# Optimization experiments

Measured on AMD Instinct MI355X. Metric: run time of the kernel, lower is better.

## Reference

```python
import jax, jax.numpy as jnp
import numpy as np

ROPE_THETA = 10000.0

def rope(x):
    # RoPE over the FULL model_dim (applied pre head-split, as in the source),
    # interleaved even/odd pairs. x: [B, S, D]
    B, S, D = x.shape
    half = D // 2
    inv_freq = 1.0 / (ROPE_THETA ** (jnp.arange(half, dtype=jnp.float32) * 2.0 / D))
    ang = jnp.arange(S, dtype=jnp.float32)[:, None] * inv_freq[None, :]  # [S, half]
    cos, sin = jnp.cos(ang), jnp.sin(ang)
    x1, x2 = x[..., 0::2], x[..., 1::2]
    r1 = x1 * cos - x2 * sin
    r2 = x1 * sin + x2 * cos
    return jnp.stack([r1, r2], axis=-1).reshape(B, S, D)


def setup_inputs() -> dict:
    key = jax.random.key(0)
    ks = jax.random.split(key, 9)
    B, S, D = 4, 2048, 768
    w = 0.02
    return {
        "X":  jax.random.normal(ks[0], (B, S, D), dtype=jnp.float32),
        "Wq": jax.random.normal(ks[1], (D, D), dtype=jnp.float32) * w,
        "bq": jnp.zeros((D,), dtype=jnp.float32),
        "Wk": jax.random.normal(ks[2], (D, D), dtype=jnp.float32) * w,
        "bk": jnp.zeros((D,), dtype=jnp.float32),
        "Wv": jax.random.normal(ks[3], (D, D), dtype=jnp.float32) * w,
        "bv": jnp.zeros((D,), dtype=jnp.float32),
        "Wo": jax.random.normal(ks[4], (D, D), dtype=jnp.float32) * w,
        "bo": jnp.zeros((D,), dtype=jnp.float32),
    }


def reference(X, Wq, bq, Wk, bk, Wv, bv, Wo, bo):
    NUM_HEADS = 12
    B, S, D = X.shape
    hd = D // NUM_HEADS

    q = rope(X @ Wq + bq)   # RoPE applied pre-split on full model_dim
    k = rope(X @ Wk + bk)
    v = X @ Wv + bv

    # Contiguous per-head slices == reshape to [B, S, H, hd]
    qh = q.reshape(B, S, NUM_HEADS, hd)
    kh = k.reshape(B, S, NUM_HEADS, hd)
    vh = v.reshape(B, S, NUM_HEADS, hd)

    scores = jnp.einsum('bqhd,bkhd->bhqk', qh, kh) / jnp.sqrt(jnp.float32(hd))
    causal = jnp.tril(jnp.ones((S, S), dtype=bool))
    scores = jnp.where(causal[None, None, :, :], scores, -jnp.inf)
    weights = jax.nn.softmax(scores, axis=-1)
    out = jnp.einsum('bhqk,bkhd->bqhd', weights, vh).reshape(B, S, D)
    return out @ Wo + bo
```

## Files before the change

### kernel.cpp

```cpp
#include <hip/hip_runtime.h>
#include <math.h>

#define D_MODEL 768
#define NUM_HEADS 12
#define HEAD_DIM 64
#define SEQ 2048
#define BATCH 4
#define MROWS (BATCH * SEQ)
#define HALF_D (D_MODEL / 2)

typedef __bf16 bf16x8 __attribute__((ext_vector_type(8)));
typedef __bf16 bf16x4 __attribute__((ext_vector_type(4)));
typedef float  f32x4  __attribute__((ext_vector_type(4)));

__device__ __forceinline__ void gload_lds16(const void* gp, void* lp) {
    __builtin_amdgcn_global_load_lds(
        (const __attribute__((address_space(1))) unsigned int*)gp,
        (__attribute__((address_space(3))) unsigned int*)lp, 16, 0, 0);
}

__global__ __launch_bounds__(256)
void rope_table(float2* __restrict__ tab)
{
    int idx = blockIdx.x * 256 + threadIdx.x;
    int s = idx / HALF_D;
    int j = idx - s * HALF_D;
    float freq = __expf(-(float)j * (9.210340371976184f / 384.0f));
    float ang  = (float)s * freq;
    float sn, cs;
    sincosf(ang, &sn, &cs);
    tab[idx] = make_float2(cs, sn);
}

__global__ __launch_bounds__(256)
void cast_x(const float* __restrict__ X, __bf16* __restrict__ Xb)
{
    size_t i = ((size_t)blockIdx.x * 256 + threadIdx.x) * 8;
    float4 u = *(const float4*)(X + i);
    float4 v = *(const float4*)(X + i + 4);
    bf16x8 o;
    o[0]=(__bf16)u.x; o[1]=(__bf16)u.y; o[2]=(__bf16)u.z; o[3]=(__bf16)u.w;
    o[4]=(__bf16)v.x; o[5]=(__bf16)v.y; o[6]=(__bf16)v.z; o[7]=(__bf16)v.w;
    *(bf16x8*)(Xb + i) = o;
}

__global__ __launch_bounds__(256)
void wcast(const float* __restrict__ W0, const float* __restrict__ W1,
           const float* __restrict__ W2, const float* __restrict__ W3,
           __bf16* __restrict__ T0, __bf16* __restrict__ T1,
           __bf16* __restrict__ T2, __bf16* __restrict__ T3)
{
    __shared__ float t[64][65];
    const int z = blockIdx.z;
    const float* W = z == 0 ? W0 : z == 1 ? W1 : z == 2 ? W2 : W3;
    __bf16*      T = z == 0 ? T0 : z == 1 ? T1 : z == 2 ? T2 : T3;

    const int tid = threadIdx.x;
    const int r0 = blockIdx.y * 64, c0 = blockIdx.x * 64;
    const int lx = tid & 63, g = tid >> 6;

    #pragma unroll
    for (int rr = 0; rr < 16; ++rr) {
        int r = g * 16 + rr;
        t[r][lx] = W[(size_t)(r0 + r) * D_MODEL + c0 + lx];
    }
    __syncthreads();

    const int n  = tid >> 2;
    const int kb = (tid & 3) * 16;
    bf16x8 o1, o2;
    #pragma unroll
    for (int m = 0; m < 8; ++m) o1[m] = (__bf16)t[kb + m][n];
    #pragma unroll
    for (int m = 0; m < 8; ++m) o2[m] = (__bf16)t[kb + 8 + m][n];
    __bf16* dst = T + (size_t)(c0 + n) * D_MODEL + r0 + kb;
    *(bf16x8*)dst       = o1;
    *(bf16x8*)(dst + 8) = o2;
}

__global__ __launch_bounds__(256)
void qkv_gemm(const __bf16* __restrict__ Xb,
              const __bf16* __restrict__ Wqt, const __bf16* __restrict__ Wkt,
              const __bf16* __restrict__ Wvt,
              const float* __restrict__ bq, const float* __restrict__ bk,
              const float* __restrict__ bv,
              const float2* __restrict__ tab,
              __bf16* __restrict__ Qb, __bf16* __restrict__ Kb,
              __bf16* __restrict__ Vtb)
{
    __shared__ bf16x8 Asf[2][8][64];
    __shared__ bf16x8 Bsf[2][8][64];

    const int tid  = threadIdx.x;
    const int wv   = tid >> 6;
    const int ln   = tid & 63;
    const int t15  = ln & 15;
    const int quad = ln >> 4;
    const int wr = wv >> 1, wc = wv & 1;

    const int lin = blockIdx.x;
    const int c   = lin >> 6;
    const int r   = lin & 63;
    const int which = c / 6;
    const int col0  = (c % 6) * 128;
    const int row0  = r * 128;

    const __bf16* Wt  = which == 0 ? Wqt : which == 1 ? Wkt : Wvt;
    const float* bias = which == 0 ? bq  : which == 1 ? bk  : bv;

    f32x4 acc[4][4];
    #pragma unroll
    for (int i = 0; i < 4; ++i)
        #pragma unroll
        for (int j = 0; j < 4; ++j) acc[i][j] = (f32x4){0.f,0.f,0.f,0.f};

    const __bf16* a0 = Xb + (size_t)(row0 + 16 * wv       + t15) * D_MODEL + 8 * quad;
    const __bf16* a1 = Xb + (size_t)(row0 + 16 * (wv + 4) + t15) * D_MODEL + 8 * quad;
    const __bf16* b0 = Wt + (size_t)(col0 + 16 * wv       + t15) * D_MODEL + 8 * quad;
    const __bf16* b1 = Wt + (size_t)(col0 + 16 * (wv + 4) + t15) * D_MODEL + 8 * quad;

    for (int k0 = 0; k0 < D_MODEL; k0 += 64) {
        __syncthreads();
        #pragma unroll
        for (int ks = 0; ks < 2; ++ks) {
            const int kk = k0 + 32 * ks;
            gload_lds16(a0 + kk, &Asf[ks][wv][0]);
            gload_lds16(a1 + kk, &Asf[ks][wv + 4][0]);
            gload_lds16(b0 + kk, &Bsf[ks][wv][0]);
            gload_lds16(b1 + kk, &Bsf[ks][wv + 4][0]);
        }
        __syncthreads();

        #pragma unroll
        for (int ks = 0; ks < 2; ++ks) {
            bf16x8 af[4], bfr[4];
            #pragma unroll
            for (int i = 0; i < 4; ++i) af[i]  = Asf[ks][4 * wr + i][ln];
            #pragma unroll
            for (int j = 0; j < 4; ++j) bfr[j] = Bsf[ks][4 * wc + j][ln];
            #pragma unroll
            for (int i = 0; i < 4; ++i)
                #pragma unroll
                for (int j = 0; j < 4; ++j)
                    acc[i][j] = __builtin_amdgcn_mfma_f32_16x16x32_bf16(af[i], bfr[j], acc[i][j], 0, 0, 0);
        }
    }

    #pragma unroll
    for (int i = 0; i < 4; ++i) {
        const int rowb = row0 + 64 * wr + 16 * i + 4 * quad;
        #pragma unroll
        for (int j = 0; j < 4; ++j) {
            const int col = col0 + 64 * wc + 16 * j + t15;
            const float bval = bias[col];
            if (which < 2) {
                const int jh  = col >> 1;
                const float sgn = (col & 1) ? 1.0f : -1.0f;
                const float oscale = (which == 0) ? 0.125f : 1.0f;
                __bf16* dst = (which ? Kb : Qb);
                #pragma unroll
                for (int rr = 0; rr < 4; ++rr) {
                    const int rw = rowb + rr;
                    const int s  = rw & (SEQ - 1);
                    float val  = acc[i][j][rr] + bval;
                    float part = __shfl_xor(val, 1, 64);
                    float2 cs  = tab[(size_t)s * HALF_D + jh];
                    dst[(size_t)rw * D_MODEL + col] = (__bf16)((val * cs.x + part * sgn * cs.y) * oscale);
                }
            } else {
                const int h = col >> 6, d = col & 63;
                const int bidx = rowb >> 11, s = rowb & (SEQ - 1);
                bf16x4 pk;
                #pragma unroll
                for (int rr = 0; rr < 4; ++rr) pk[rr] = (__bf16)(acc[i][j][rr] + bval);
                *(bf16x4*)(Vtb + ((size_t)(bidx * NUM_HEADS + h) * 64 + d) * SEQ + s) = pk;
            }
        }
    }
}

__global__ __launch_bounds__(256)
void out_gemm(const __bf16* __restrict__ Ab, const __bf16* __restrict__ Wt,
              const float* __restrict__ bias, float* __restrict__ Cout)
{
    __shared__ bf16x8 Asf[2][8][64];
    __shared__ bf16x8 Bsf[2][8][64];

    const int tid  = threadIdx.x;
    const int wv   = tid >> 6;
    const int ln   = tid & 63;
    const int t15  = ln & 15;
    const int quad = ln >> 4;
    const int wr = wv >> 1, wc = wv & 1;

    const int lin = blockIdx.x;
    const int col0 = (lin >> 6) * 128;
    const int row0 = (lin & 63) * 128;

    f32x4 acc[4][4];
    #pragma unroll
    for (int i = 0; i < 4; ++i)
        #pragma unroll
        for (int j = 0; j < 4; ++j) acc[i][j] = (f32x4){0.f,0.f,0.f,0.f};

    const __bf16* a0 = Ab + (size_t)(row0 + 16 * wv       + t15) * D_MODEL + 8 * quad;
    const __bf16* a1 = Ab + (size_t)(row0 + 16 * (wv + 4) + t15) * D_MODEL + 8 * quad;
    const __bf16* b0 = Wt + (size_t)(col0 + 16 * wv       + t15) * D_MODEL + 8 * quad;
    const __bf16* b1 = Wt + (size_t)(col0 + 16 * (wv + 4) + t15) * D_MODEL + 8 * quad;

    for (int k0 = 0; k0 < D_MODEL; k0 += 64) {
        __syncthreads();
        #pragma unroll
        for (int ks = 0; ks < 2; ++ks) {
            const int kk = k0 + 32 * ks;
            gload_lds16(a0 + kk, &Asf[ks][wv][0]);
            gload_lds16(a1 + kk, &Asf[ks][wv + 4][0]);
            gload_lds16(b0 + kk, &Bsf[ks][wv][0]);
            gload_lds16(b1 + kk, &Bsf[ks][wv + 4][0]);
        }
        __syncthreads();

        #pragma unroll
        for (int ks = 0; ks < 2; ++ks) {
            bf16x8 af[4], bfr[4];
            #pragma unroll
            for (int i = 0; i < 4; ++i) af[i]  = Asf[ks][4 * wr + i][ln];
            #pragma unroll
            for (int j = 0; j < 4; ++j) bfr[j] = Bsf[ks][4 * wc + j][ln];
            #pragma unroll
            for (int i = 0; i < 4; ++i)
                #pragma unroll
                for (int j = 0; j < 4; ++j)
                    acc[i][j] = __builtin_amdgcn_mfma_f32_16x16x32_bf16(af[i], bfr[j], acc[i][j], 0, 0, 0);
        }
    }

    #pragma unroll
    for (int i = 0; i < 4; ++i) {
        const int rowb = row0 + 64 * wr + 16 * i + 4 * quad;
        #pragma unroll
        for (int j = 0; j < 4; ++j) {
            const int col = col0 + 64 * wc + 16 * j + t15;
            const float bval = bias[col];
            #pragma unroll
            for (int rr = 0; rr < 4; ++rr)
                Cout[(size_t)(rowb + rr) * D_MODEL + col] = acc[i][j][rr] + bval;
        }
    }
}

__device__ __forceinline__ void attn_tile(
    const bf16x8 (*Kbuf)[64], const bf16x8 (*Vbuf)[64],
    __bf16 (*Psw)[72],
    bf16x8 aq0, bf16x8 aq1,
    f32x4* o, float* lacc,
    int ln, int t15, int quad, int j0, int qabs, bool domask)
{
    f32x4 s[4];
    #pragma unroll
    for (int c = 0; c < 4; ++c) {
        s[c] = (f32x4){0.f, 0.f, 0.f, 0.f};
        s[c] = __builtin_amdgcn_mfma_f32_16x16x32_bf16(aq0, Kbuf[c][ln],     s[c], 0, 0, 0);
        s[c] = __builtin_amdgcn_mfma_f32_16x16x32_bf16(aq1, Kbuf[4 + c][ln], s[c], 0, 0, 0);
    }

    float p[4][4];
    #pragma unroll
    for (int c = 0; c < 4; ++c)
        #pragma unroll
        for (int r = 0; r < 4; ++r) {
            float e = __expf(s[c][r]);
            if (domask && (j0 + 16 * c + t15 > qabs + r)) e = 0.f;
            p[c][r] = e;
            lacc[r] += e;
        }

    #pragma unroll
    for (int c = 0; c < 4; ++c)
        #pragma unroll
        for (int r = 0; r < 4; ++r)
            Psw[4 * quad + r][16 * c + t15] = (__bf16)p[c][r];
    __asm__ volatile("s_waitcnt lgkmcnt(0)" ::: "memory");

    bf16x8 ap0 = *(const bf16x8*)&Psw[t15][8 * quad];
    bf16x8 ap1 = *(const bf16x8*)&Psw[t15][32 + 8 * quad];

    #pragma unroll
    for (int c = 0; c < 4; ++c) {
        o[c] = __builtin_amdgcn_mfma_f32_16x16x32_bf16(ap0, Vbuf[c][ln],     o[c], 0, 0, 0);
        o[c] = __builtin_amdgcn_mfma_f32_16x16x32_bf16(ap1, Vbuf[4 + c][ln], o[c], 0, 0, 0);
    }
}

__global__ __launch_bounds__(512)
void attn_flash(const __bf16* __restrict__ Q, const __bf16* __restrict__ K,
                const __bf16* __restrict__ Vt, __bf16* __restrict__ O)
{
    __shared__ bf16x8 Kf[2][8][64];
    __shared__ bf16x8 Vf[2][8][64];
    __shared__ __bf16 Psb[8][16][72];

    const int tid  = threadIdx.x;
    const int wv   = tid >> 6;
    const int ln   = tid & 63;
    const int t15  = ln & 15;
    const int quad = ln >> 4;

    const int n  = blockIdx.x;
    const int sb = n >> 8;
    const int tb = n & 255;
    const int a  = tb & 15;
    const int qt = (sb == 0) ? a : (sb == 1) ? (15 - a) : ((a + 8) & 15);
    const int bh = (tb >> 4) + 16 * sb;
    const int b  = bh / NUM_HEADS;
    const int h  = bh % NUM_HEADS;
    const int q0 = qt * 128;
    const int nt = (q0 >> 6) + 2;

    bf16x8 aq0, aq1;
    {
        const __bf16* qs = Q + (size_t)(b * SEQ + q0 + 16 * wv + t15) * D_MODEL + h * 64 + 8 * quad;
        aq0 = *(const bf16x8*)qs;
        aq1 = *(const bf16x8*)(qs + 32);
    }

    const __bf16* kp = K  + ((size_t)b * SEQ + 16 * (wv & 3) + t15) * D_MODEL
                          + h * 64 + 32 * (wv >> 2) + 8 * quad;
    const __bf16* vp = Vt + ((size_t)bh * 64 + 16 * (wv & 3) + t15) * SEQ
                          + 32 * (wv >> 2) + 8 * quad;

    f32x4 o[4];
    #pragma unroll
    for (int c = 0; c < 4; ++c) o[c] = (f32x4){0.f,0.f,0.f,0.f};
    float lacc[4] = {0.f, 0.f, 0.f, 0.f};
    const int qabs = q0 + 16 * wv + 4 * quad;

    gload_lds16(kp, &Kf[0][wv][0]);
    gload_lds16(vp, &Vf[0][wv][0]);

    int cur = 0;
    for (int it = 0; it < nt; ++it) {
        __syncthreads();
        if (it + 1 < nt) {
            const int jn = (it + 1) * 64;
            gload_lds16(kp + (size_t)jn * D_MODEL, &Kf[cur ^ 1][wv][0]);
            gload_lds16(vp + jn,                   &Vf[cur ^ 1][wv][0]);
        }
        const int j0 = it * 64;
        const bool domask = (j0 + 63) > (q0 + 16 * wv);
        attn_tile(Kf[cur], Vf[cur], Psb[wv], aq0, aq1, o, lacc,
                  ln, t15, quad, j0, qabs, domask);
        cur ^= 1;
    }

    #pragma unroll
    for (int off = 1; off < 16; off <<= 1)
        #pragma unroll
        for (int r = 0; r < 4; ++r)
            lacc[r] += __shfl_xor(lacc[r], off, 64);

    float inv[4];
    #pragma unroll
    for (int r = 0; r < 4; ++r) inv[r] = 1.0f / lacc[r];
    #pragma unroll
    for (int c = 0; c < 4; ++c)
        #pragma unroll
        for (int r = 0; r < 4; ++r) {
            int row = qabs + r;
            O[(size_t)(b * SEQ + row) * D_MODEL + h * 64 + 16 * c + t15] = (__bf16)(o[c][r] * inv[r]);
        }
}

extern "C" void kernel_launch(void* const* d_in, const int* in_sizes, int n_in,
                              void* d_out, int out_size, void* d_ws, size_t ws_size,
                              hipStream_t stream) {
    const float* X  = (const float*)d_in[0];
    const float* Wq = (const float*)d_in[1];
    const float* bq = (const float*)d_in[2];
    const float* Wk = (const float*)d_in[3];
    const float* bk = (const float*)d_in[4];
    const float* Wv = (const float*)d_in[5];
    const float* bv = (const float*)d_in[6];
    const float* Wo = (const float*)d_in[7];
    const float* bo = (const float*)d_in[8];
    float* out = (float*)d_out;

    const size_t BSD = (size_t)MROWS * D_MODEL;
    const size_t WSZ = (size_t)D_MODEL * D_MODEL;

    __bf16* Xb  = (__bf16*)d_ws;
    __bf16* Qb  = Xb  + BSD;
    __bf16* Kb  = Qb  + BSD;
    __bf16* Vtb = Kb  + BSD;
    __bf16* Ob  = Vtb + BSD;
    __bf16* Wqt = Ob  + BSD;
    __bf16* Wkt = Wqt + WSZ;
    __bf16* Wvt = Wkt + WSZ;
    __bf16* Wot = Wvt + WSZ;
    float2* Tab = (float2*)(Wot + WSZ);

    rope_table<<<(SEQ * HALF_D) / 256, 256, 0, stream>>>(Tab);
    cast_x<<<BSD / (256 * 8), 256, 0, stream>>>(X, Xb);
    wcast<<<dim3(12, 12, 4), 256, 0, stream>>>(Wq, Wk, Wv, Wo, Wqt, Wkt, Wvt, Wot);

    qkv_gemm<<<1152, 256, 0, stream>>>(Xb, Wqt, Wkt, Wvt, bq, bk, bv, Tab, Qb, Kb, Vtb);

    attn_flash<<<768, 512, 0, stream>>>(Qb, Kb, Vtb, Ob);

    out_gemm<<<384, 256, 0, stream>>>(Ob, Wot, bo, out);
}
```

Measured before the change: 275.1 us.

## Restructure QKV GEMM to stage full-K A tile in LDS and stream B from registers

The QKV projection GEMM now uses 32x256 output tiles. Each block loads its whole 32-row by 768-K slab of X into LDS once, behind a single barrier. Each wave then streams its 64 columns of the transposed weight straight from global memory into registers with a three-slot prefetch ring, which removes the per-K-step LDS round trips and barriers. The grid doubles to 2304 blocks. In exchange, A-tile reuse per weight load drops and each block holds 48 KB of LDS, which may limit occupancy, and weight reads now rely on cache rather than shared staging.

Measured after the change: 312.5 us. +13.6%, slower.

```diff
diff --git a/kernel.cpp b/kernel.cpp
--- a/kernel.cpp
+++ b/kernel.cpp
@@ -88,70 +88,74 @@
               __bf16* __restrict__ Qb, __bf16* __restrict__ Kb,
               __bf16* __restrict__ Vtb)
 {
-    __shared__ bf16x8 Asf[2][8][64];
-    __shared__ bf16x8 Bsf[2][8][64];
+    __shared__ bf16x8 Af[48][64];
 
     const int tid  = threadIdx.x;
     const int wv   = tid >> 6;
     const int ln   = tid & 63;
     const int t15  = ln & 15;
     const int quad = ln >> 4;
-    const int wr = wv >> 1, wc = wv & 1;
-
-    const int lin = blockIdx.x;
-    const int c   = lin >> 6;
-    const int r   = lin & 63;
-    const int which = c / 6;
-    const int col0  = (c % 6) * 128;
-    const int row0  = r * 128;
+
+    const int lin  = blockIdx.x;
+    const int c    = lin >> 8;
+    const int r    = lin & 255;
+    const int which = c / 3;
+    const int col0  = (c % 3) * 256;
+    const int row0  = r * 32;
 
     const __bf16* Wt  = which == 0 ? Wqt : which == 1 ? Wkt : Wvt;
     const float* bias = which == 0 ? bq  : which == 1 ? bk  : bv;
 
-    f32x4 acc[4][4];
-    #pragma unroll
-    for (int i = 0; i < 4; ++i)
+    #pragma unroll
+    for (int cc = 0; cc < 12; ++cc) {
+        const int id = wv * 12 + cc;
+        const int s  = id >> 1;
+        const int i  = id & 1;
+        const __bf16* src = Xb + (size_t)(row0 + 16 * i + t15) * D_MODEL + 32 * s + 8 * quad;
+        gload_lds16(src, &Af[id][0]);
+    }
+    __syncthreads();
+
+    const __bf16* Bbase = Wt + (size_t)(col0 + 64 * wv + t15) * D_MODEL + 8 * quad;
+
+    f32x4 acc[2][4];
+    #pragma unroll
+    for (int i = 0; i < 2; ++i)
         #pragma unroll
         for (int j = 0; j < 4; ++j) acc[i][j] = (f32x4){0.f,0.f,0.f,0.f};
 
-    const __bf16* a0 = Xb + (size_t)(row0 + 16 * wv       + t15) * D_MODEL + 8 * quad;
-    const __bf16* a1 = Xb + (size_t)(row0 + 16 * (wv + 4) + t15) * D_MODEL + 8 * quad;
-    const __bf16* b0 = Wt + (size_t)(col0 + 16 * wv       + t15) * D_MODEL + 8 * quad;
-    const __bf16* b1 = Wt + (size_t)(col0 + 16 * (wv + 4) + t15) * D_MODEL + 8 * quad;
-
-    for (int k0 = 0; k0 < D_MODEL; k0 += 64) {
-        __syncthreads();
-        #pragma unroll
-        for (int ks = 0; ks < 2; ++ks) {
-            const int kk = k0 + 32 * ks;
-            gload_lds16(a0 + kk, &Asf[ks][wv][0]);
-            gload_lds16(a1 + kk, &Asf[ks][wv + 4][0]);
-            gload_lds16(b0 + kk, &Bsf[ks][wv][0]);
-            gload_lds16(b1 + kk, &Bsf[ks][wv + 4][0]);
-        }
-        __syncthreads();
-
-        #pragma unroll
-        for (int ks = 0; ks < 2; ++ks) {
-            bf16x8 af[4], bfr[4];
+    bf16x8 bfr[3][4];
+    #pragma unroll
+    for (int j = 0; j < 4; ++j) {
+        bfr[0][j] = *(const bf16x8*)(Bbase + (size_t)(16 * j) * D_MODEL);
+        bfr[1][j] = *(const bf16x8*)(Bbase + (size_t)(16 * j) * D_MODEL + 32);
+    }
+
+    #pragma unroll
+    for (int s = 0; s < 24; ++s) {
+        const int cur = s % 3;
+        if (s + 2 < 24) {
+            const int kn = (s + 2) * 32;
+            const int nb = (s + 2) % 3;
             #pragma unroll
-            for (int i = 0; i < 4; ++i) af[i]  = Asf[ks][4 * wr + i][ln];
-            #pragma unroll
-            for (int j = 0; j < 4; ++j) bfr[j] = Bsf[ks][4 * wc + j][ln];
-            #pragma unroll
-            for (int i = 0; i < 4; ++i)
-                #pragma unroll
-                for (int j = 0; j < 4; ++j)
-                    acc[i][j] = __builtin_amdgcn_mfma_f32_16x16x32_bf16(af[i], bfr[j], acc[i][j], 0, 0, 0);
-        }
-    }
-
-    #pragma unroll
-    for (int i = 0; i < 4; ++i) {
-        const int rowb = row0 + 64 * wr + 16 * i + 4 * quad;
+            for (int j = 0; j < 4; ++j)
+                bfr[nb][j] = *(const bf16x8*)(Bbase + (size_t)(16 * j) * D_MODEL + kn);
+        }
+        bf16x8 af0 = Af[2 * s][ln];
+        bf16x8 af1 = Af[2 * s + 1][ln];
         #pragma unroll
         for (int j = 0; j < 4; ++j) {
-            const int col = col0 + 64 * wc + 16 * j + t15;
+            acc[0][j] = __builtin_amdgcn_mfma_f32_16x16x32_bf16(af0, bfr[cur][j], acc[0][j], 0, 0, 0);
+            acc[1][j] = __builtin_amdgcn_mfma_f32_16x16x32_bf16(af1, bfr[cur][j], acc[1][j], 0, 0, 0);
+        }
+    }
+
+    #pragma unroll
+    for (int i = 0; i < 2; ++i) {
+        const int rowb = row0 + 16 * i + 4 * quad;
+        #pragma unroll
+        for (int j = 0; j < 4; ++j) {
+            const int col = col0 + 64 * wv + 16 * j + t15;
             const float bval = bias[col];
             if (which < 2) {
                 const int jh  = col >> 1;
@@ -403,7 +407,7 @@
     cast_x<<<BSD / (256 * 8), 256, 0, stream>>>(X, Xb);
     wcast<<<dim3(12, 12, 4), 256, 0, stream>>>(Wq, Wk, Wv, Wo, Wqt, Wkt, Wvt, Wot);
 
-    qkv_gemm<<<1152, 256, 0, stream>>>(Xb, Wqt, Wkt, Wvt, bq, bk, bv, Tab, Qb, Kb, Vtb);
+    qkv_gemm<<<2304, 256, 0, stream>>>(Xb, Wqt, Wkt, Wvt, bq, bk, bv, Tab, Qb, Kb, Vtb);
 
     attn_flash<<<768, 512, 0, stream>>>(Qb, Kb, Vtb, Ob);
 
```

## Merge prep kernels, reorder attention blocks longest-first, skip fully masked warp tiles

Applied to the files above, without the earlier changes.

Combines the rope table, X cast and weight transpose-cast into one launch so two kernel launches and their gaps go away. The attention grid now maps blocks to query tiles in longest-first order (qt descending), replacing the previous interleaved scheme, so heavy causal tiles start early and tail imbalance shrinks. Each wave also skips attn_tile for key tiles that lie entirely beyond its last query row, removing wasted MMA work in the diagonal tiles. The skip sits inside a loop with __syncthreads, but the barrier is still reached by all waves, so correctness holds.

Result: faster. 264.0 us (-4.0%).

```diff
diff --git a/kernel.cpp b/kernel.cpp
--- a/kernel.cpp
+++ b/kernel.cpp
@@ -20,62 +20,62 @@
 }
 
 __global__ __launch_bounds__(256)
-void rope_table(float2* __restrict__ tab)
-{
-    int idx = blockIdx.x * 256 + threadIdx.x;
-    int s = idx / HALF_D;
-    int j = idx - s * HALF_D;
-    float freq = __expf(-(float)j * (9.210340371976184f / 384.0f));
-    float ang  = (float)s * freq;
-    float sn, cs;
-    sincosf(ang, &sn, &cs);
-    tab[idx] = make_float2(cs, sn);
-}
-
-__global__ __launch_bounds__(256)
-void cast_x(const float* __restrict__ X, __bf16* __restrict__ Xb)
-{
-    size_t i = ((size_t)blockIdx.x * 256 + threadIdx.x) * 8;
-    float4 u = *(const float4*)(X + i);
-    float4 v = *(const float4*)(X + i + 4);
-    bf16x8 o;
-    o[0]=(__bf16)u.x; o[1]=(__bf16)u.y; o[2]=(__bf16)u.z; o[3]=(__bf16)u.w;
-    o[4]=(__bf16)v.x; o[5]=(__bf16)v.y; o[6]=(__bf16)v.z; o[7]=(__bf16)v.w;
-    *(bf16x8*)(Xb + i) = o;
-}
-
-__global__ __launch_bounds__(256)
-void wcast(const float* __restrict__ W0, const float* __restrict__ W1,
-           const float* __restrict__ W2, const float* __restrict__ W3,
-           __bf16* __restrict__ T0, __bf16* __restrict__ T1,
-           __bf16* __restrict__ T2, __bf16* __restrict__ T3)
+void prep(const float* __restrict__ X, __bf16* __restrict__ Xb,
+          const float* __restrict__ W0, const float* __restrict__ W1,
+          const float* __restrict__ W2, const float* __restrict__ W3,
+          __bf16* __restrict__ T0, __bf16* __restrict__ T1,
+          __bf16* __restrict__ T2, __bf16* __restrict__ T3,
+          float2* __restrict__ tab)
 {
     __shared__ float t[64][65];
-    const int z = blockIdx.z;
-    const float* W = z == 0 ? W0 : z == 1 ? W1 : z == 2 ? W2 : W3;
-    __bf16*      T = z == 0 ? T0 : z == 1 ? T1 : z == 2 ? T2 : T3;
-
+    const int n   = blockIdx.x;
     const int tid = threadIdx.x;
-    const int r0 = blockIdx.y * 64, c0 = blockIdx.x * 64;
-    const int lx = tid & 63, g = tid >> 6;
-
-    #pragma unroll
-    for (int rr = 0; rr < 16; ++rr) {
-        int r = g * 16 + rr;
-        t[r][lx] = W[(size_t)(r0 + r) * D_MODEL + c0 + lx];
-    }
-    __syncthreads();
-
-    const int n  = tid >> 2;
-    const int kb = (tid & 3) * 16;
-    bf16x8 o1, o2;
-    #pragma unroll
-    for (int m = 0; m < 8; ++m) o1[m] = (__bf16)t[kb + m][n];
-    #pragma unroll
-    for (int m = 0; m < 8; ++m) o2[m] = (__bf16)t[kb + 8 + m][n];
-    __bf16* dst = T + (size_t)(c0 + n) * D_MODEL + r0 + kb;
-    *(bf16x8*)dst       = o1;
-    *(bf16x8*)(dst + 8) = o2;
+
+    if (n < 3072) {
+        int idx = n * 256 + tid;
+        int s = idx / HALF_D;
+        int j = idx - s * HALF_D;
+        float freq = __expf(-(float)j * (9.210340371976184f / 384.0f));
+        float sn, cs;
+        sincosf((float)s * freq, &sn, &cs);
+        tab[idx] = make_float2(cs, sn);
+    } else if (n < 6144) {
+        size_t i = ((size_t)(n - 3072) * 256 + tid) * 8;
+        float4 u = *(const float4*)(X + i);
+        float4 v = *(const float4*)(X + i + 4);
+        bf16x8 o;
+        o[0]=(__bf16)u.x; o[1]=(__bf16)u.y; o[2]=(__bf16)u.z; o[3]=(__bf16)u.w;
+        o[4]=(__bf16)v.x; o[5]=(__bf16)v.y; o[6]=(__bf16)v.z; o[7]=(__bf16)v.w;
+        *(bf16x8*)(Xb + i) = o;
+    } else {
+        int m = n - 6144;
+        int z = m / 144;
+        int rem = m - z * 144;
+        int by = rem / 12, bx = rem % 12;
+        const float* W = z == 0 ? W0 : z == 1 ? W1 : z == 2 ? W2 : W3;
+        __bf16*      T = z == 0 ? T0 : z == 1 ? T1 : z == 2 ? T2 : T3;
+
+        const int r0 = by * 64, c0 = bx * 64;
+        const int lx = tid & 63, g = tid >> 6;
+
+        #pragma unroll
+        for (int rr = 0; rr < 16; ++rr) {
+            int r = g * 16 + rr;
+            t[r][lx] = W[(size_t)(r0 + r) * D_MODEL + c0 + lx];
+        }
+        __syncthreads();
+
+        const int nn = tid >> 2;
+        const int kb = (tid & 3) * 16;
+        bf16x8 o1, o2;
+        #pragma unroll
+        for (int mm = 0; mm < 8; ++mm) o1[mm] = (__bf16)t[kb + mm][nn];
+        #pragma unroll
+        for (int mm = 0; mm < 8; ++mm) o2[mm] = (__bf16)t[kb + 8 + mm][nn];
+        __bf16* dst = T + (size_t)(c0 + nn) * D_MODEL + r0 + kb;
+        *(bf16x8*)dst       = o1;
+        *(bf16x8*)(dst + 8) = o2;
+    }
 }
 
 __global__ __launch_bounds__(256)
@@ -307,11 +307,8 @@
     const int quad = ln >> 4;
 
     const int n  = blockIdx.x;
-    const int sb = n >> 8;
-    const int tb = n & 255;
-    const int a  = tb & 15;
-    const int qt = (sb == 0) ? a : (sb == 1) ? (15 - a) : ((a + 8) & 15);
-    const int bh = (tb >> 4) + 16 * sb;
+    const int qt = 15 - (n / 48);
+    const int bh = n % 48;
     const int b  = bh / NUM_HEADS;
     const int h  = bh % NUM_HEADS;
     const int q0 = qt * 128;
@@ -334,6 +331,7 @@
     for (int c = 0; c < 4; ++c) o[c] = (f32x4){0.f,0.f,0.f,0.f};
     float lacc[4] = {0.f, 0.f, 0.f, 0.f};
     const int qabs = q0 + 16 * wv + 4 * quad;
+    const int wmax = q0 + 16 * wv + 15;
 
     gload_lds16(kp, &Kf[0][wv][0]);
     gload_lds16(vp, &Vf[0][wv][0]);
@@ -347,9 +345,11 @@
             gload_lds16(vp + jn,                   &Vf[cur ^ 1][wv][0]);
         }
         const int j0 = it * 64;
-        const bool domask = (j0 + 63) > (q0 + 16 * wv);
-        attn_tile(Kf[cur], Vf[cur], Psb[wv], aq0, aq1, o, lacc,
-                  ln, t15, quad, j0, qabs, domask);
+        if (j0 <= wmax) {
+            const bool domask = (j0 + 63) > (q0 + 16 * wv);
+            attn_tile(Kf[cur], Vf[cur], Psb[wv], aq0, aq1, o, lacc,
+                      ln, t15, quad, j0, qabs, domask);
+        }
         cur ^= 1;
     }
 
@@ -399,9 +399,7 @@
     __bf16* Wot = Wvt + WSZ;
     float2* Tab = (float2*)(Wot + WSZ);
 
-    rope_table<<<(SEQ * HALF_D) / 256, 256, 0, stream>>>(Tab);
-    cast_x<<<BSD / (256 * 8), 256, 0, stream>>>(X, Xb);
-    wcast<<<dim3(12, 12, 4), 256, 0, stream>>>(Wq, Wk, Wv, Wo, Wqt, Wkt, Wvt, Wot);
+    prep<<<6720, 256, 0, stream>>>(X, Xb, Wq, Wk, Wv, Wo, Wqt, Wkt, Wvt, Wot, Tab);
 
     qkv_gemm<<<1152, 256, 0, stream>>>(Xb, Wqt, Wkt, Wvt, bq, bk, bv, Tab, Qb, Kb, Vtb);
 
```
